# Optimization experiments

Measured on AMD Instinct MI355X. Metric: run time of the kernel, lower is better.

The kernel has to match this reference:

```python
import jax, jax.numpy as jnp
import numpy as np

N = 8192
E = 262144
D_IN = 256
D_OUT = 256

def setup_inputs() -> dict:
    key = jax.random.key(0)
    k1, k2, k3, k4 = jax.random.split(key, 4)
    x = jax.random.normal(k1, (N, D_IN), dtype=jnp.float32)
    edge_index = jax.random.randint(k2, (2, E), 0, N, dtype=jnp.int64)
    W = jax.random.normal(k3, (D_OUT, D_IN), dtype=jnp.float32) * (1.0 / np.sqrt(D_IN))
    b = jax.random.normal(k4, (D_OUT,), dtype=jnp.float32) * 0.01
    return {"x": x, "edge_index": edge_index, "W": W, "b": b}

def reference(x, edge_index, W, b):
    num_nodes = x.shape[0]
    # dense adjacency: adj[src, dst] = 1.0 (duplicates collapse to 1, matching torch assignment)
    adj = jnp.zeros((num_nodes, num_nodes), dtype=x.dtype)
    adj = adj.at[edge_index[0], edge_index[1]].set(1.0)
    adj = adj + jnp.eye(num_nodes, dtype=x.dtype)  # self-loops (may yield 2.0 if edge had self-loop, as in torch)
    deg = adj.sum(axis=1, keepdims=True)           # [N, 1]
    adj_norm = adj / deg                           # row-normalized
    aggregated = adj_norm @ x                      # [N, D_IN]
    return aggregated @ W.T + b                    # linear: [N, D_OUT]
```

## Files before the change

kernel.cpp:

```cpp
#include <hip/hip_runtime.h>
#include <hip/hip_fp16.h>


#define NNODES 8192
#define DFEAT  256
#define MAXDEG 192
#define GEMMB  512
#define POISON 0xAAAAAAAAu
#define LPAD   72
#define HSLOTS 256

typedef __attribute__((ext_vector_type(8))) _Float16 f16x8;
typedef __attribute__((ext_vector_type(4))) _Float16 f16x4;
typedef __attribute__((ext_vector_type(4))) float    f32x4;
typedef __attribute__((ext_vector_type(4))) unsigned u32x4;

__global__ __launch_bounds__(256) void gcn_gemm_scatter(
    const float* __restrict__ X, const float* __restrict__ W,
    const int* __restrict__ ei, int E,
    _Float16* __restrict__ Y, unsigned* __restrict__ deg,
    unsigned short* __restrict__ adj) {
  const int bid = blockIdx.x, tid = threadIdx.x;

  if (bid >= GEMMB) {
    int e = (bid - GEMMB) * 256 + tid;
    if (e < E) {
      int s = ei[e];
      int d = ei[E + e];
      unsigned pos = atomicAdd(&deg[s], 1u) - POISON;
      if (pos < MAXDEG) adj[(size_t)s * MAXDEG + pos] = (unsigned short)d;
    }
    return;
  }

  const int wave = tid >> 6, lane = tid & 63;
  const int R0 = (bid >> 2) * 64, C0 = (bid & 3) * 64;
  const int lr = lane & 15, kh = (lane >> 4) * 8;

  f32x4 acc[4];
#pragma unroll
  for (int i = 0; i < 4; ++i) acc[i] = (f32x4){0.f, 0.f, 0.f, 0.f};

  const float* ap = X + (size_t)(R0 + wave * 16 + lr) * DFEAT + kh;
  const float* wp = W + (size_t)(C0 + lr) * DFEAT + kh;

#pragma unroll
  for (int k0 = 0; k0 < DFEAT; k0 += 32) {
    float4 x0 = *(const float4*)(ap + k0);
    float4 x1 = *(const float4*)(ap + k0 + 4);
    f16x8 a = {(_Float16)x0.x, (_Float16)x0.y, (_Float16)x0.z, (_Float16)x0.w,
               (_Float16)x1.x, (_Float16)x1.y, (_Float16)x1.z, (_Float16)x1.w};
#pragma unroll
    for (int nt = 0; nt < 4; ++nt) {
      float4 w0 = *(const float4*)(wp + k0 + nt * 16 * DFEAT);
      float4 w1 = *(const float4*)(wp + k0 + nt * 16 * DFEAT + 4);
      f16x8 bh = {(_Float16)w0.x, (_Float16)w0.y, (_Float16)w0.z, (_Float16)w0.w,
                  (_Float16)w1.x, (_Float16)w1.y, (_Float16)w1.z, (_Float16)w1.w};
      f16x8 bl = {(_Float16)(w0.x - (float)bh[0]), (_Float16)(w0.y - (float)bh[1]),
                  (_Float16)(w0.z - (float)bh[2]), (_Float16)(w0.w - (float)bh[3]),
                  (_Float16)(w1.x - (float)bh[4]), (_Float16)(w1.y - (float)bh[5]),
                  (_Float16)(w1.z - (float)bh[6]), (_Float16)(w1.w - (float)bh[7])};
      acc[nt] = __builtin_amdgcn_mfma_f32_16x16x32_f16(a, bh, acc[nt], 0, 0, 0);
      acc[nt] = __builtin_amdgcn_mfma_f32_16x16x32_f16(a, bl, acc[nt], 0, 0, 0);
    }
  }

  __shared__ __align__(16) _Float16 tile[64][LPAD];
  const int rbase = wave * 16 + (lane >> 4) * 4;
#pragma unroll
  for (int nt = 0; nt < 4; ++nt)
#pragma unroll
    for (int r = 0; r < 4; ++r)
      tile[rbase + r][nt * 16 + lr] = (_Float16)acc[nt][r];
  __syncthreads();

#pragma unroll
  for (int it = 0; it < 2; ++it) {
    int c = tid + it * 256;
    int row = c >> 3, seg = c & 7;
    u32x4 v = *(const u32x4*)&tile[row][seg * 8];
    __builtin_nontemporal_store(
        v, (u32x4*)(Y + (size_t)(R0 + row) * DFEAT + C0 + seg * 8));
  }
}

__global__ __launch_bounds__(256) void gcn_aggregate(
    const unsigned* __restrict__ deg, const unsigned short* __restrict__ adj,
    const _Float16* __restrict__ Y, const float* __restrict__ bias,
    float* __restrict__ out) {
  __shared__ unsigned       tabS[4][HSLOTS];
  __shared__ unsigned short listS[4][MAXDEG];
  __shared__ int            cntS[4];

  const int tid = threadIdx.x;
  const int wave = tid >> 6, lane = tid & 63;
  const int node = blockIdx.x * 4 + wave;
  unsigned*       tab  = tabS[wave];
  unsigned short* list = listS[wave];

  int d = (int)(deg[node] - POISON);
  if (d > MAXDEG) d = MAXDEG;

#pragma unroll
  for (int i = 0; i < HSLOTS / 64; ++i) tab[lane + i * 64] = 0xFFFFFFFFu;
  if (lane == 0) cntS[wave] = 0;
  __syncthreads();

  for (int r0 = 0; r0 < d; r0 += 64) {
    int idx = r0 + lane;
    if (idx < d) {
      unsigned v = (unsigned)adj[(size_t)node * MAXDEG + idx];
      unsigned h = (v * 2654435761u) >> 24;
      while (true) {
        unsigned old = atomicCAS(&tab[h], 0xFFFFFFFFu, v);
        if (old == 0xFFFFFFFFu) {
          int p = atomicAdd(&cntS[wave], 1);
          list[p] = (unsigned short)v;
          break;
        }
        if (old == v) break;
        h = (h + 1) & (HSLOTS - 1);
      }
    }
  }
  __syncthreads();

  const int n = cntS[wave];
  const int ch4 = lane * 4;

  f16x4 sv = *(const f16x4*)(Y + (size_t)node * DFEAT + ch4);
  float ax = (float)sv[0], ay = (float)sv[1], az = (float)sv[2], aw = (float)sv[3];
  float bx = 0.f, by = 0.f, bz = 0.f, bw = 0.f;

  int k = 0;
  for (; k + 4 <= n; k += 4) {
    int j0 = list[k], j1 = list[k + 1], j2 = list[k + 2], j3 = list[k + 3];
    f16x4 r0 = *(const f16x4*)(Y + (size_t)j0 * DFEAT + ch4);
    f16x4 r1 = *(const f16x4*)(Y + (size_t)j1 * DFEAT + ch4);
    f16x4 r2 = *(const f16x4*)(Y + (size_t)j2 * DFEAT + ch4);
    f16x4 r3 = *(const f16x4*)(Y + (size_t)j3 * DFEAT + ch4);
    ax += (float)r0[0] + (float)r1[0]; bx += (float)r2[0] + (float)r3[0];
    ay += (float)r0[1] + (float)r1[1]; by += (float)r2[1] + (float)r3[1];
    az += (float)r0[2] + (float)r1[2]; bz += (float)r2[2] + (float)r3[2];
    aw += (float)r0[3] + (float)r1[3]; bw += (float)r2[3] + (float)r3[3];
  }
  for (; k < n; ++k) {
    f16x4 r0 = *(const f16x4*)(Y + (size_t)list[k] * DFEAT + ch4);
    ax += (float)r0[0]; ay += (float)r0[1];
    az += (float)r0[2]; aw += (float)r0[3];
  }

  const float inv = 1.f / (float)(n + 1);
  const float4 b4 = *(const float4*)(bias + ch4);
  f32x4 o;
  o[0] = (ax + bx) * inv + b4.x;
  o[1] = (ay + by) * inv + b4.y;
  o[2] = (az + bz) * inv + b4.z;
  o[3] = (aw + bw) * inv + b4.w;
  __builtin_nontemporal_store(o, (f32x4*)(out + (size_t)node * DFEAT + ch4));
}

extern "C" void kernel_launch(void* const* d_in, const int* in_sizes, int n_in,
                              void* d_out, int out_size, void* d_ws, size_t ws_size,
                              hipStream_t stream) {
  const float* x  = (const float*)d_in[0];
  const int*   ei = (const int*)d_in[1];
  const float* W  = (const float*)d_in[2];
  const float* b  = (const float*)d_in[3];
  float* out = (float*)d_out;
  const int E = in_sizes[1] / 2;

  char* p = (char*)d_ws;
  size_t off = 0;
  auto take = [&](size_t bytes) { char* r = p + off; off = (off + bytes + 255) & ~(size_t)255; return r; };
  unsigned*       deg = (unsigned*)       take((size_t)NNODES * 4);
  unsigned short* adj = (unsigned short*) take((size_t)NNODES * MAXDEG * 2);
  _Float16*       Y   = (_Float16*)       take((size_t)NNODES * DFEAT * 2);

  const int nbs = (E + 255) / 256;
  gcn_gemm_scatter<<<GEMMB + nbs, 256, 0, stream>>>(x, W, ei, E, Y, deg, adj);
  gcn_aggregate<<<NNODES / 4, 256, 0, stream>>>(deg, adj, Y, b, out);
}
```

Measured before the change: 101.0 us.

## Fuse GEMM/scatter and aggregation into one persistent cooperative kernel with grid sync

```diff
diff --git a/kernel.cpp b/kernel.cpp
--- a/kernel.cpp
+++ b/kernel.cpp
@@ -1,163 +1,168 @@
 #include <hip/hip_runtime.h>
 #include <hip/hip_fp16.h>
+#include <hip/hip_cooperative_groups.h>
 
 
 #define NNODES 8192
 #define DFEAT  256
 #define MAXDEG 192
 #define GEMMB  512
+#define SCATB  1024
+#define AGGB   2048
 #define POISON 0xAAAAAAAAu
 #define LPAD   72
 #define HSLOTS 256
+
+namespace cg = cooperative_groups;
 
 typedef __attribute__((ext_vector_type(8))) _Float16 f16x8;
 typedef __attribute__((ext_vector_type(4))) _Float16 f16x4;
 typedef __attribute__((ext_vector_type(4))) float    f32x4;
 typedef __attribute__((ext_vector_type(4))) unsigned u32x4;
 
-__global__ __launch_bounds__(256) void gcn_gemm_scatter(
+__global__ void gcn_fused(
     const float* __restrict__ X, const float* __restrict__ W,
     const int* __restrict__ ei, int E,
     _Float16* __restrict__ Y, unsigned* __restrict__ deg,
-    unsigned short* __restrict__ adj) {
-  const int bid = blockIdx.x, tid = threadIdx.x;
-
-  if (bid >= GEMMB) {
-    int e = (bid - GEMMB) * 256 + tid;
-    if (e < E) {
-      int s = ei[e];
-      int d = ei[E + e];
-      unsigned pos = atomicAdd(&deg[s], 1u) - POISON;
-      if (pos < MAXDEG) adj[(size_t)s * MAXDEG + pos] = (unsigned short)d;
-    }
-    return;
-  }
-
+    unsigned short* __restrict__ adj, const float* __restrict__ bias,
+    float* __restrict__ out) {
+  const int tid = threadIdx.x;
   const int wave = tid >> 6, lane = tid & 63;
-  const int R0 = (bid >> 2) * 64, C0 = (bid & 3) * 64;
-  const int lr = lane & 15, kh = (lane >> 4) * 8;
-
-  f32x4 acc[4];
-#pragma unroll
-  for (int i = 0; i < 4; ++i) acc[i] = (f32x4){0.f, 0.f, 0.f, 0.f};
-
-  const float* ap = X + (size_t)(R0 + wave * 16 + lr) * DFEAT + kh;
-  const float* wp = W + (size_t)(C0 + lr) * DFEAT + kh;
-
-#pragma unroll
-  for (int k0 = 0; k0 < DFEAT; k0 += 32) {
-    float4 x0 = *(const float4*)(ap + k0);
-    float4 x1 = *(const float4*)(ap + k0 + 4);
-    f16x8 a = {(_Float16)x0.x, (_Float16)x0.y, (_Float16)x0.z, (_Float16)x0.w,
-               (_Float16)x1.x, (_Float16)x1.y, (_Float16)x1.z, (_Float16)x1.w};
-#pragma unroll
-    for (int nt = 0; nt < 4; ++nt) {
-      float4 w0 = *(const float4*)(wp + k0 + nt * 16 * DFEAT);
-      float4 w1 = *(const float4*)(wp + k0 + nt * 16 * DFEAT + 4);
-      f16x8 bh = {(_Float16)w0.x, (_Float16)w0.y, (_Float16)w0.z, (_Float16)w0.w,
-                  (_Float16)w1.x, (_Float16)w1.y, (_Float16)w1.z, (_Float16)w1.w};
-      f16x8 bl = {(_Float16)(w0.x - (float)bh[0]), (_Float16)(w0.y - (float)bh[1]),
-                  (_Float16)(w0.z - (float)bh[2]), (_Float16)(w0.w - (float)bh[3]),
-                  (_Float16)(w1.x - (float)bh[4]), (_Float16)(w1.y - (float)bh[5]),
-                  (_Float16)(w1.z - (float)bh[6]), (_Float16)(w1.w - (float)bh[7])};
-      acc[nt] = __builtin_amdgcn_mfma_f32_16x16x32_f16(a, bh, acc[nt], 0, 0, 0);
-      acc[nt] = __builtin_amdgcn_mfma_f32_16x16x32_f16(a, bl, acc[nt], 0, 0, 0);
-    }
-  }
 
   __shared__ __align__(16) _Float16 tile[64][LPAD];
-  const int rbase = wave * 16 + (lane >> 4) * 4;
-#pragma unroll
-  for (int nt = 0; nt < 4; ++nt)
-#pragma unroll
-    for (int r = 0; r < 4; ++r)
-      tile[rbase + r][nt * 16 + lr] = (_Float16)acc[nt][r];
-  __syncthreads();
-
-#pragma unroll
-  for (int it = 0; it < 2; ++it) {
-    int c = tid + it * 256;
-    int row = c >> 3, seg = c & 7;
-    u32x4 v = *(const u32x4*)&tile[row][seg * 8];
-    __builtin_nontemporal_store(
-        v, (u32x4*)(Y + (size_t)(R0 + row) * DFEAT + C0 + seg * 8));
-  }
-}
-
-__global__ __launch_bounds__(256) void gcn_aggregate(
-    const unsigned* __restrict__ deg, const unsigned short* __restrict__ adj,
-    const _Float16* __restrict__ Y, const float* __restrict__ bias,
-    float* __restrict__ out) {
   __shared__ unsigned       tabS[4][HSLOTS];
   __shared__ unsigned short listS[4][MAXDEG];
   __shared__ int            cntS[4];
 
-  const int tid = threadIdx.x;
-  const int wave = tid >> 6, lane = tid & 63;
-  const int node = blockIdx.x * 4 + wave;
-  unsigned*       tab  = tabS[wave];
-  unsigned short* list = listS[wave];
+  for (int u = blockIdx.x; u < GEMMB + SCATB; u += gridDim.x) {
+    if (u >= GEMMB) {
+      int e = (u - GEMMB) * 256 + tid;
+      if (e < E) {
+        int s = ei[e];
+        int d = ei[E + e];
+        unsigned pos = atomicAdd(&deg[s], 1u) - POISON;
+        if (pos < MAXDEG) adj[(size_t)s * MAXDEG + pos] = (unsigned short)d;
+      }
+      continue;
+    }
+    const int R0 = (u >> 2) * 64, C0 = (u & 3) * 64;
+    const int lr = lane & 15, kh = (lane >> 4) * 8;
 
-  int d = (int)(deg[node] - POISON);
-  if (d > MAXDEG) d = MAXDEG;
+    f32x4 acc[4];
+#pragma unroll
+    for (int i = 0; i < 4; ++i) acc[i] = (f32x4){0.f, 0.f, 0.f, 0.f};
+
+    const float* ap = X + (size_t)(R0 + wave * 16 + lr) * DFEAT + kh;
+    const float* wp = W + (size_t)(C0 + lr) * DFEAT + kh;
 
 #pragma unroll
-  for (int i = 0; i < HSLOTS / 64; ++i) tab[lane + i * 64] = 0xFFFFFFFFu;
-  if (lane == 0) cntS[wave] = 0;
-  __syncthreads();
-
-  for (int r0 = 0; r0 < d; r0 += 64) {
-    int idx = r0 + lane;
-    if (idx < d) {
-      unsigned v = (unsigned)adj[(size_t)node * MAXDEG + idx];
-      unsigned h = (v * 2654435761u) >> 24;
-      while (true) {
-        unsigned old = atomicCAS(&tab[h], 0xFFFFFFFFu, v);
-        if (old == 0xFFFFFFFFu) {
-          int p = atomicAdd(&cntS[wave], 1);
-          list[p] = (unsigned short)v;
-          break;
-        }
-        if (old == v) break;
-        h = (h + 1) & (HSLOTS - 1);
+    for (int k0 = 0; k0 < DFEAT; k0 += 32) {
+      float4 x0 = *(const float4*)(ap + k0);
+      float4 x1 = *(const float4*)(ap + k0 + 4);
+      f16x8 a = {(_Float16)x0.x, (_Float16)x0.y, (_Float16)x0.z, (_Float16)x0.w,
+                 (_Float16)x1.x, (_Float16)x1.y, (_Float16)x1.z, (_Float16)x1.w};
+#pragma unroll
+      for (int nt = 0; nt < 4; ++nt) {
+        float4 w0 = *(const float4*)(wp + k0 + nt * 16 * DFEAT);
+        float4 w1 = *(const float4*)(wp + k0 + nt * 16 * DFEAT + 4);
+        f16x8 bh = {(_Float16)w0.x, (_Float16)w0.y, (_Float16)w0.z, (_Float16)w0.w,
+                    (_Float16)w1.x, (_Float16)w1.y, (_Float16)w1.z, (_Float16)w1.w};
+        f16x8 bl = {(_Float16)(w0.x - (float)bh[0]), (_Float16)(w0.y - (float)bh[1]),
+                    (_Float16)(w0.z - (float)bh[2]), (_Float16)(w0.w - (float)bh[3]),
+                    (_Float16)(w1.x - (float)bh[4]), (_Float16)(w1.y - (float)bh[5]),
+                    (_Float16)(w1.z - (float)bh[6]), (_Float16)(w1.w - (float)bh[7])};
+        acc[nt] = __builtin_amdgcn_mfma_f32_16x16x32_f16(a, bh, acc[nt], 0, 0, 0);
+        acc[nt] = __builtin_amdgcn_mfma_f32_16x16x32_f16(a, bl, acc[nt], 0, 0, 0);
       }
     }
-  }
-  __syncthreads();
 
-  const int n = cntS[wave];
-  const int ch4 = lane * 4;
+    __syncthreads();
+    const int rbase = wave * 16 + (lane >> 4) * 4;
+#pragma unroll
+    for (int nt = 0; nt < 4; ++nt)
+#pragma unroll
+      for (int r = 0; r < 4; ++r)
+        tile[rbase + r][nt * 16 + lr] = (_Float16)acc[nt][r];
+    __syncthreads();
 
-  f16x4 sv = *(const f16x4*)(Y + (size_t)node * DFEAT + ch4);
-  float ax = (float)sv[0], ay = (float)sv[1], az = (float)sv[2], aw = (float)sv[3];
-  float bx = 0.f, by = 0.f, bz = 0.f, bw = 0.f;
-
-  int k = 0;
-  for (; k + 4 <= n; k += 4) {
-    int j0 = list[k], j1 = list[k + 1], j2 = list[k + 2], j3 = list[k + 3];
-    f16x4 r0 = *(const f16x4*)(Y + (size_t)j0 * DFEAT + ch4);
-    f16x4 r1 = *(const f16x4*)(Y + (size_t)j1 * DFEAT + ch4);
-    f16x4 r2 = *(const f16x4*)(Y + (size_t)j2 * DFEAT + ch4);
-    f16x4 r3 = *(const f16x4*)(Y + (size_t)j3 * DFEAT + ch4);
-    ax += (float)r0[0] + (float)r1[0]; bx += (float)r2[0] + (float)r3[0];
-    ay += (float)r0[1] + (float)r1[1]; by += (float)r2[1] + (float)r3[1];
-    az += (float)r0[2] + (float)r1[2]; bz += (float)r2[2] + (float)r3[2];
-    aw += (float)r0[3] + (float)r1[3]; bw += (float)r2[3] + (float)r3[3];
-  }
-  for (; k < n; ++k) {
-    f16x4 r0 = *(const f16x4*)(Y + (size_t)list[k] * DFEAT + ch4);
-    ax += (float)r0[0]; ay += (float)r0[1];
-    az += (float)r0[2]; aw += (float)r0[3];
+#pragma unroll
+    for (int it = 0; it < 2; ++it) {
+      int c = tid + it * 256;
+      int row = c >> 3, seg = c & 7;
+      u32x4 v = *(const u32x4*)&tile[row][seg * 8];
+      *(u32x4*)(Y + (size_t)(R0 + row) * DFEAT + C0 + seg * 8) = v;
+    }
   }
 
-  const float inv = 1.f / (float)(n + 1);
-  const float4 b4 = *(const float4*)(bias + ch4);
-  f32x4 o;
-  o[0] = (ax + bx) * inv + b4.x;
-  o[1] = (ay + by) * inv + b4.y;
-  o[2] = (az + bz) * inv + b4.z;
-  o[3] = (aw + bw) * inv + b4.w;
-  __builtin_nontemporal_store(o, (f32x4*)(out + (size_t)node * DFEAT + ch4));
+  cg::this_grid().sync();
+
+  for (int u = blockIdx.x; u < AGGB; u += gridDim.x) {
+    const int node = u * 4 + wave;
+    unsigned*       tab  = tabS[wave];
+    unsigned short* list = listS[wave];
+
+    int d = (int)(deg[node] - POISON);
+    if (d > MAXDEG) d = MAXDEG;
+
+#pragma unroll
+    for (int i = 0; i < HSLOTS / 64; ++i) tab[lane + i * 64] = 0xFFFFFFFFu;
+    if (lane == 0) cntS[wave] = 0;
+    __syncthreads();
+
+    for (int r0 = 0; r0 < d; r0 += 64) {
+      int idx = r0 + lane;
+      if (idx < d) {
+        unsigned v = (unsigned)adj[(size_t)node * MAXDEG + idx];
+        unsigned h = (v * 2654435761u) >> 24;
+        while (true) {
+          unsigned old = atomicCAS(&tab[h], 0xFFFFFFFFu, v);
+          if (old == 0xFFFFFFFFu) {
+            int p = atomicAdd(&cntS[wave], 1);
+            list[p] = (unsigned short)v;
+            break;
+          }
+          if (old == v) break;
+          h = (h + 1) & (HSLOTS - 1);
+        }
+      }
+    }
+    __syncthreads();
+
+    const int n = cntS[wave];
+    const int ch4 = lane * 4;
+
+    f16x4 sv = *(const f16x4*)(Y + (size_t)node * DFEAT + ch4);
+    float ax = (float)sv[0], ay = (float)sv[1], az = (float)sv[2], aw = (float)sv[3];
+    float bx = 0.f, by = 0.f, bz = 0.f, bw = 0.f;
+
+    int k = 0;
+    for (; k + 4 <= n; k += 4) {
+      int j0 = list[k], j1 = list[k + 1], j2 = list[k + 2], j3 = list[k + 3];
+      f16x4 r0 = *(const f16x4*)(Y + (size_t)j0 * DFEAT + ch4);
+      f16x4 r1 = *(const f16x4*)(Y + (size_t)j1 * DFEAT + ch4);
+      f16x4 r2 = *(const f16x4*)(Y + (size_t)j2 * DFEAT + ch4);
+      f16x4 r3 = *(const f16x4*)(Y + (size_t)j3 * DFEAT + ch4);
+      ax += (float)r0[0] + (float)r1[0]; bx += (float)r2[0] + (float)r3[0];
+      ay += (float)r0[1] + (float)r1[1]; by += (float)r2[1] + (float)r3[1];
+      az += (float)r0[2] + (float)r1[2]; bz += (float)r2[2] + (float)r3[2];
+      aw += (float)r0[3] + (float)r1[3]; bw += (float)r2[3] + (float)r3[3];
+    }
+    for (; k < n; ++k) {
+      f16x4 r0 = *(const f16x4*)(Y + (size_t)list[k] * DFEAT + ch4);
+      ax += (float)r0[0]; ay += (float)r0[1];
+      az += (float)r0[2]; aw += (float)r0[3];
+    }
+
+    const float inv = 1.f / (float)(n + 1);
+    const float4 b4 = *(const float4*)(bias + ch4);
+    f32x4 o;
+    o[0] = (ax + bx) * inv + b4.x;
+    o[1] = (ay + by) * inv + b4.y;
+    o[2] = (az + bz) * inv + b4.z;
+    o[3] = (aw + bw) * inv + b4.w;
+    __builtin_nontemporal_store(o, (f32x4*)(out + (size_t)node * DFEAT + ch4));
+    __syncthreads();
+  }
 }
 
 extern "C" void kernel_launch(void* const* d_in, const int* in_sizes, int n_in,
@@ -168,7 +173,7 @@
   const float* W  = (const float*)d_in[2];
   const float* b  = (const float*)d_in[3];
   float* out = (float*)d_out;
-  const int E = in_sizes[1] / 2;
+  int E = in_sizes[1] / 2;
 
   char* p = (char*)d_ws;
   size_t off = 0;
@@ -177,7 +182,14 @@
   unsigned short* adj = (unsigned short*) take((size_t)NNODES * MAXDEG * 2);
   _Float16*       Y   = (_Float16*)       take((size_t)NNODES * DFEAT * 2);
 
-  const int nbs = (E + 255) / 256;
-  gcn_gemm_scatter<<<GEMMB + nbs, 256, 0, stream>>>(x, W, ei, E, Y, deg, adj);
-  gcn_aggregate<<<NNODES / 4, 256, 0, stream>>>(deg, adj, Y, b, out);
+  int maxb = 0;
+  hipOccupancyMaxActiveBlocksPerMultiprocessor(&maxb, (const void*)gcn_fused, 256, 0);
+  if (maxb < 1) maxb = 1;
+  int nblk = maxb * 256;
+  if (nblk > AGGB) nblk = AGGB;
+
+  void* args[] = {(void*)&x, (void*)&W, (void*)&ei, (void*)&E, (void*)&Y,
+                  (void*)&deg, (void*)&adj, (void*)&b, (void*)&out};
+  hipLaunchCooperativeKernel((const void*)gcn_fused, dim3(nblk), dim3(256),
+                             args, 0, stream);
 }
```

New measurement: 196.9 us. 1.95x slower.
